# Kernel tuning notes

Measured on AMD Instinct MI355X. Metric: run time of the kernel, lower is better.

## Reference

```python
import jax, jax.numpy as jnp
import numpy as np

HIDDEN = 1024
HEADS = 16
HEAD = HIDDEN // HEADS
EXPAND = 4096
EPS = 1e-5


def layer_norm(x, g, b):
    mu = jnp.mean(x, axis=-1, keepdims=True)
    var = jnp.mean((x - mu) ** 2, axis=-1, keepdims=True)
    return (x - mu) * jax.lax.rsqrt(var + EPS) * g + b


def setup_inputs() -> dict:
    key = jax.random.key(0)
    ks = jax.random.split(key, 12)
    s = 0.02
    return {
        "x": jax.random.normal(ks[0], (4, 2048, HIDDEN), dtype=jnp.float32),
        "Wqkv": jax.random.normal(ks[1], (HIDDEN, 3 * HIDDEN), dtype=jnp.float32) * s,
        "bqkv": jnp.zeros((3 * HIDDEN,), jnp.float32),
        "Wproj": jax.random.normal(ks[2], (HIDDEN, HIDDEN), dtype=jnp.float32) * s,
        "bproj": jnp.zeros((HIDDEN,), jnp.float32),
        "W1": jax.random.normal(ks[3], (HIDDEN, EXPAND), dtype=jnp.float32) * s,
        "b1": jnp.zeros((EXPAND,), jnp.float32),
        "W2": jax.random.normal(ks[4], (EXPAND, HIDDEN), dtype=jnp.float32) * s,
        "b2": jnp.zeros((HIDDEN,), jnp.float32),
        "g1": jnp.ones((HIDDEN,), jnp.float32),
        "be1": jnp.zeros((HIDDEN,), jnp.float32),
        "g2": jnp.ones((HIDDEN,), jnp.float32),
        "be2": jnp.zeros((HIDDEN,), jnp.float32),
    }


def attention(x, Wqkv, bqkv, Wproj, bproj):
    B, L, _ = x.shape
    qkv = (x @ Wqkv + bqkv).reshape(B, L, 3, HEADS, HEAD)
    q, k, v = [qkv[:, :, i].transpose(0, 2, 1, 3) for i in range(3)]  # [B,H,L,D]
    attn = jnp.einsum("bnld,bnkd->bnlk", q, k) / np.sqrt(HEAD).astype(np.float32)
    attn = jax.nn.softmax(attn, axis=-1)
    o = jnp.einsum("bnlk,bnkd->bnld", attn, v)
    o = o.transpose(0, 2, 1, 3).reshape(B, L, HIDDEN)
    return o @ Wproj + bproj


def reference(x, Wqkv, bqkv, Wproj, bproj, W1, b1, W2, b2, g1, be1, g2, be2):
    # post-norm transformer block (pre_norm=False), dropout=0 (eval)
    h = layer_norm(x + attention(x, Wqkv, bqkv, Wproj, bproj), g1, be1)
    ff = jax.nn.gelu(h @ W1 + b1, approximate=False) @ W2 + b2
    return layer_norm(h + ff, g2, be2)
```

## Files before the change

### kernel.cpp

```cpp
#include <hip/hip_runtime.h>
#include <hip/hip_bf16.h>
#include <math.h>


typedef __bf16 bf16_t;
typedef __bf16 bf16x8 __attribute__((ext_vector_type(8)));
typedef __bf16 bf16x4 __attribute__((ext_vector_type(4)));
typedef float f32x4 __attribute__((ext_vector_type(4)));
typedef float f32x16 __attribute__((ext_vector_type(16)));

#define HID   1024
#define NHEAD 16
#define HD    64
#define EXPD  4096
#define LSEQ  2048
#define BATCH 4
#define MROWS (BATCH * LSEQ)

#if __has_builtin(__builtin_amdgcn_exp2f)
#define EXP2F __builtin_amdgcn_exp2f
#else
#define EXP2F exp2f
#endif

__device__ __forceinline__ void gld_lds16(const bf16_t* g, bf16_t* l) {
  __builtin_amdgcn_global_load_lds(
      (const __attribute__((address_space(1))) void*)g,
      (__attribute__((address_space(3))) void*)l, 16, 0, 0);
}

__device__ __forceinline__ void swap32(unsigned& a, unsigned& b) {
#if __has_builtin(__builtin_amdgcn_permlane32_swap)
  auto r = __builtin_amdgcn_permlane32_swap(a, b, false, false);
  a = r[0]; b = r[1];
#else
  bool hiL = ((threadIdx.x & 63) >= 32);
  unsigned pa = (unsigned)__shfl_xor((int)a, 32, 64);
  unsigned pb = (unsigned)__shfl_xor((int)b, 32, 64);
  unsigned na = hiL ? pb : a;
  unsigned nb = hiL ? b : pa;
  a = na; b = nb;
#endif
}

__device__ __forceinline__ unsigned pk_bf16(float lo, float hi) {
  bf16_t l = (bf16_t)lo, h = (bf16_t)hi;
  unsigned short ul, uh;
  __builtin_memcpy(&ul, &l, 2);
  __builtin_memcpy(&uh, &h, 2);
  return (unsigned)ul | ((unsigned)uh << 16);
}

__global__ __launch_bounds__(256) void cvt_bf16(const float* __restrict__ in,
                                                bf16_t* __restrict__ out, int n4) {
  int i = blockIdx.x * 256 + threadIdx.x;
  if (i >= n4) return;
  float4 v = ((const float4*)in)[i];
  bf16x4 o;
  o[0] = (bf16_t)v.x; o[1] = (bf16_t)v.y; o[2] = (bf16_t)v.z; o[3] = (bf16_t)v.w;
  ((bf16x4*)out)[i] = o;
}

__global__ __launch_bounds__(256) void transpose_cvt(const float* __restrict__ W,
                                                     bf16_t* __restrict__ Wt,
                                                     int K, int N) {
  __shared__ float tile[32][33];
  int n0 = blockIdx.x * 32, k0 = blockIdx.y * 32;
  int tx = threadIdx.x & 31, ty = threadIdx.x >> 5;
#pragma unroll
  for (int i = 0; i < 32; i += 8)
    tile[ty + i][tx] = W[(size_t)(k0 + ty + i) * N + n0 + tx];
  __syncthreads();
#pragma unroll
  for (int i = 0; i < 32; i += 8)
    Wt[(size_t)(n0 + ty + i) * K + k0 + tx] = (bf16_t)tile[tx][ty + i];
}

__global__ __launch_bounds__(256) void transpose_v(const bf16_t* __restrict__ qkvb,
                                                   bf16_t* __restrict__ vT) {
  __shared__ bf16_t tile[64][65];
  const int l0 = blockIdx.x * 64;
  const int bh = blockIdx.y;
  const int b = bh >> 4, h = bh & 15;
  const int tx = threadIdx.x & 63, ty = threadIdx.x >> 6;
  const bf16_t* src = qkvb + ((size_t)(b * LSEQ + l0)) * 3072 + 2048 + h * 64;
#pragma unroll
  for (int i = 0; i < 16; ++i) {
    int l = ty + 4 * i;
    tile[l][tx] = src[(size_t)l * 3072 + tx];
  }
  __syncthreads();
  bf16_t* dst = vT + ((size_t)bh * HD) * LSEQ + l0;
#pragma unroll
  for (int i = 0; i < 16; ++i) {
    int d = ty + 4 * i;
    dst[(size_t)d * LSEQ + tx] = tile[tx][d];
  }
}

__global__ __launch_bounds__(256) void gemm_bt(const bf16_t* __restrict__ A,
                                               const bf16_t* __restrict__ Bt,
                                               const float* __restrict__ bias,
                                               void* __restrict__ C,
                                               int M, int N, int K, int mode) {
  __shared__ bf16_t As[128 * 32];
  __shared__ bf16_t Bs[128 * 32];
  const int nbx = gridDim.x;
  int p = blockIdx.y * nbx + blockIdx.x;
  const int GM = 8;
  int group = p / (GM * nbx);
  int idx = p - group * (GM * nbx);
  const int by = group * GM + (idx & (GM - 1));
  const int bx = idx >> 3;
  const int n0 = bx * 128, m0 = by * 128;

  const int t = threadIdx.x;
  const int lane = t & 63, w = t >> 6;
  const int wr = w >> 1, wc = w & 1;
  const int quad = lane >> 4, l16 = lane & 15;

  f32x4 acc[4][4];
#pragma unroll
  for (int i = 0; i < 4; ++i)
#pragma unroll
    for (int j = 0; j < 4; ++j) acc[i][j] = (f32x4){0.f, 0.f, 0.f, 0.f};

  const int r0 = t >> 2;
  const unsigned ksw = (((unsigned)t & 3u) ^ ((unsigned)(r0 >> 1) & 3u)) * 8u;
  const unsigned offL0 = (unsigned)r0 * (unsigned)K + ksw;
  const unsigned offL1 = offL0 + 64u * (unsigned)K;

  const bf16_t* aK = A + (size_t)m0 * K;
  const bf16_t* bK = Bt + (size_t)n0 * K;

  for (int k0 = 0; k0 < K; k0 += 32) {
    gld_lds16(aK + offL0, As + t * 8);
    gld_lds16(aK + offL1, As + (t + 256) * 8);
    gld_lds16(bK + offL0, Bs + t * 8);
    gld_lds16(bK + offL1, Bs + (t + 256) * 8);
    aK += 32;
    bK += 32;
    __syncthreads();
    bf16x8 af[4], bfr[4];
#pragma unroll
    for (int i = 0; i < 4; ++i) {
      int row = wr * 64 + 16 * i + l16;
      int pos = row * 4 + (quad ^ ((row >> 1) & 3));
      af[i] = *(const bf16x8*)(As + pos * 8);
    }
#pragma unroll
    for (int j = 0; j < 4; ++j) {
      int row = wc * 64 + 16 * j + l16;
      int pos = row * 4 + (quad ^ ((row >> 1) & 3));
      bfr[j] = *(const bf16x8*)(Bs + pos * 8);
    }
#pragma unroll
    for (int i = 0; i < 4; ++i)
#pragma unroll
      for (int j = 0; j < 4; ++j)
        acc[i][j] = __builtin_amdgcn_mfma_f32_16x16x32_bf16(af[i], bfr[j], acc[i][j], 0, 0, 0);
    __syncthreads();
  }

#pragma unroll
  for (int i = 0; i < 4; ++i) {
    int rowb = m0 + wr * 64 + 16 * i + quad * 4;
#pragma unroll
    for (int j = 0; j < 4; ++j) {
      int col = n0 + wc * 64 + 16 * j + l16;
      float bv = bias[col];
#pragma unroll
      for (int r = 0; r < 4; ++r) {
        float v = acc[i][j][r] + bv;
        size_t idx = (size_t)(rowb + r) * N + col;
        if (mode == 0) {
          ((bf16_t*)C)[idx] = (bf16_t)v;
        } else if (mode == 1) {
          float u = v * (0.7978845608028654f + 0.0356774081f * v * v);
          float e = EXP2F(u * 2.885390082f);
          float th = (e - 1.f) / (e + 1.f);
          float gel = 0.5f * v * (1.f + th);
          ((bf16_t*)C)[idx] = (bf16_t)gel;
        } else {
          ((float*)C)[idx] = v;
        }
      }
    }
  }
}

__global__ __launch_bounds__(256) void attn_kernel(const bf16_t* __restrict__ qkv,
                                                   const bf16_t* __restrict__ vT,
                                                   bf16_t* __restrict__ ob) {
  __shared__ bf16_t smem[3 * 128 * 64];
  bf16_t* Ks  = smem;
  bf16_t* Vts = smem + 8192;
  bf16_t* Qs  = smem + 16384;
  const int qt = blockIdx.x, h = blockIdx.y, b = blockIdx.z;
  const int t = threadIdx.x, lane = t & 63, w = t >> 6;
  const int l32 = lane & 31, hi = lane >> 5;
  const size_t RS = 3 * HID;
  const int bh = b * NHEAD + h;

  const bf16_t* qbase = qkv + ((size_t)(b * LSEQ + qt * 128)) * RS + h * HD;
  const bf16_t* kbase = qkv + ((size_t)b * LSEQ) * RS + HID + h * HD;
  const bf16_t* vtbase = vT + (size_t)bh * HD * LSEQ;

#pragma unroll
  for (int s = 0; s < 4; ++s) {
    int l = t + s * 256;
    int r = l >> 3, c8 = l & 7;
    gld_lds16(qbase + (size_t)r * RS + ((c8 ^ (r & 7)) * 8), Qs + l * 8);
  }
  __syncthreads();

  const float sc = 0.18033688011112042f;
  bf16x8 bq[4];
  {
    int qrow = 32 * w + l32;
#pragma unroll
    for (int c = 0; c < 4; ++c) {
      int y = 2 * c + hi;
      bf16x8 q8 = *(const bf16x8*)(Qs + qrow * 64 + ((y ^ (qrow & 7)) * 8));
#pragma unroll
      for (int e = 0; e < 8; ++e) q8[e] = (bf16_t)((float)q8[e] * sc);
      bq[c] = q8;
    }
  }

  f32x16 accO[2];
#pragma unroll
  for (int dt = 0; dt < 2; ++dt)
#pragma unroll
    for (int e = 0; e < 16; ++e) accO[dt][e] = 0.f;
  float l_acc = 0.f;

  for (int kt = 0; kt < LSEQ / 128; ++kt) {
    __syncthreads();
#pragma unroll
    for (int s = 0; s < 4; ++s) {
      int l = t + s * 256;
      int r = l >> 3, c8 = l & 7;
      gld_lds16(kbase + (size_t)(kt * 128 + r) * RS + ((c8 ^ (r & 7)) * 8), Ks + l * 8);
      int rv = l >> 4, c16 = l & 15;
      gld_lds16(vtbase + (size_t)rv * LSEQ + kt * 128 + ((c16 ^ (rv & 7)) * 8), Vts + l * 8);
    }
    __syncthreads();

#pragma unroll
    for (int kt2 = 0; kt2 < 2; ++kt2) {
      f32x16 s0, s1;
#pragma unroll
      for (int e = 0; e < 16; ++e) { s0[e] = 0.f; s1[e] = 0.f; }
#pragma unroll
      for (int c = 0; c < 4; ++c) {
        int y = 2 * c + hi;
        int r0 = (2 * kt2 + 0) * 32 + l32;
        bf16x8 a0 = *(const bf16x8*)(Ks + r0 * 64 + ((y ^ (r0 & 7)) * 8));
        s0 = __builtin_amdgcn_mfma_f32_32x32x16_bf16(a0, bq[c], s0, 0, 0, 0);
        int r1 = (2 * kt2 + 1) * 32 + l32;
        bf16x8 a1 = *(const bf16x8*)(Ks + r1 * 64 + ((y ^ (r1 & 7)) * 8));
        s1 = __builtin_amdgcn_mfma_f32_32x32x16_bf16(a1, bq[c], s1, 0, 0, 0);
      }

      unsigned pf[2][2][4];
#pragma unroll
      for (int tile = 0; tile < 2; ++tile) {
        f32x16& sv = tile ? s1 : s0;
        float p[16];
#pragma unroll
        for (int e = 0; e < 16; ++e) { p[e] = EXP2F(sv[e]); l_acc += p[e]; }
        unsigned lo[4], hi_[4];
#pragma unroll
        for (int g = 0; g < 4; ++g) {
          lo[g] = pk_bf16(p[4 * g + 0], p[4 * g + 1]);
          hi_[g] = pk_bf16(p[4 * g + 2], p[4 * g + 3]);
        }
#pragma unroll
        for (int c2 = 0; c2 < 2; ++c2) {
          unsigned aL = lo[2 * c2], bL = lo[2 * c2 + 1];
          swap32(aL, bL);
          pf[tile][c2][0] = aL; pf[tile][c2][2] = bL;
          unsigned aH = hi_[2 * c2], bH = hi_[2 * c2 + 1];
          swap32(aH, bH);
          pf[tile][c2][1] = aH; pf[tile][c2][3] = bH;
        }
      }

#pragma unroll
      for (int dt = 0; dt < 2; ++dt)
#pragma unroll
        for (int tile = 0; tile < 2; ++tile)
#pragma unroll
          for (int c2 = 0; c2 < 2; ++c2) {
            int ktile = 2 * kt2 + tile;
            int c8v = ktile * 4 + c2 * 2 + hi;
            int rv = dt * 32 + l32;
            bf16x8 av = *(const bf16x8*)(Vts + rv * 128 + ((c8v ^ (rv & 7)) * 8));
            union { unsigned u[4]; bf16x8 v; } bp;
            bp.u[0] = pf[tile][c2][0]; bp.u[1] = pf[tile][c2][1];
            bp.u[2] = pf[tile][c2][2]; bp.u[3] = pf[tile][c2][3];
            accO[dt] = __builtin_amdgcn_mfma_f32_32x32x16_bf16(av, bp.v, accO[dt], 0, 0, 0);
          }
    }
  }

  l_acc += __shfl_xor(l_acc, 32, 64);
  float inv = 1.f / l_acc;

  __syncthreads();
  bf16_t* Osh = smem;
  {
    int q = 32 * w + l32;
#pragma unroll
    for (int dt = 0; dt < 2; ++dt)
#pragma unroll
      for (int e = 0; e < 16; ++e) {
        int d = dt * 32 + (e & 3) + 8 * (e >> 2) + 4 * hi;
        Osh[q * 68 + d] = (bf16_t)(accO[dt][e] * inv);
      }
  }
  __syncthreads();
#pragma unroll
  for (int s = 0; s < 4; ++s) {
    int l = t + s * 256;
    int r = l >> 3, c8 = l & 7;
    bf16x8 v = *(const bf16x8*)(Osh + r * 68 + c8 * 8);
    *(bf16x8*)(ob + ((size_t)(b * LSEQ + qt * 128 + r)) * HID + h * HD + c8 * 8) = v;
  }
}

__global__ __launch_bounds__(256) void resid_ln(const float* __restrict__ X,
                                                const float* __restrict__ Y,
                                                const float* __restrict__ g,
                                                const float* __restrict__ be,
                                                float* __restrict__ outf,
                                                bf16_t* __restrict__ outb) {
  const int row = blockIdx.x;
  const int t = threadIdx.x;
  float4 a = ((const float4*)X)[(size_t)row * 256 + t];
  float4 bvec = ((const float4*)Y)[(size_t)row * 256 + t];
  float v0 = a.x + bvec.x, v1 = a.y + bvec.y, v2 = a.z + bvec.z, v3 = a.w + bvec.w;
  float s = v0 + v1 + v2 + v3;
  float s2 = v0 * v0 + v1 * v1 + v2 * v2 + v3 * v3;
#pragma unroll
  for (int msk = 1; msk < 64; msk <<= 1) {
    s += __shfl_xor(s, msk, 64);
    s2 += __shfl_xor(s2, msk, 64);
  }
  __shared__ float red[8];
  int w = t >> 6;
  if ((t & 63) == 0) { red[w] = s; red[w + 4] = s2; }
  __syncthreads();
  s = red[0] + red[1] + red[2] + red[3];
  s2 = red[4] + red[5] + red[6] + red[7];
  float mu = s * (1.f / 1024.f);
  float var = s2 * (1.f / 1024.f) - mu * mu;
  float rstd = rsqrtf(var + 1e-5f);
  float4 gg = ((const float4*)g)[t];
  float4 bb = ((const float4*)be)[t];
  float o0 = (v0 - mu) * rstd * gg.x + bb.x;
  float o1 = (v1 - mu) * rstd * gg.y + bb.y;
  float o2 = (v2 - mu) * rstd * gg.z + bb.z;
  float o3 = (v3 - mu) * rstd * gg.w + bb.w;
  float4 o = {o0, o1, o2, o3};
  ((float4*)outf)[(size_t)row * 256 + t] = o;
  if (outb) {
    bf16x4 ob4;
    ob4[0] = (bf16_t)o0; ob4[1] = (bf16_t)o1; ob4[2] = (bf16_t)o2; ob4[3] = (bf16_t)o3;
    ((bf16x4*)outb)[(size_t)row * 256 + t] = ob4;
  }
}

extern "C" void kernel_launch(void* const* d_in, const int* in_sizes, int n_in,
                              void* d_out, int out_size, void* d_ws, size_t ws_size,
                              hipStream_t stream) {
  const float* x     = (const float*)d_in[0];
  const float* Wqkv  = (const float*)d_in[1];
  const float* bqkv  = (const float*)d_in[2];
  const float* Wproj = (const float*)d_in[3];
  const float* bproj = (const float*)d_in[4];
  const float* W1    = (const float*)d_in[5];
  const float* b1    = (const float*)d_in[6];
  const float* W2    = (const float*)d_in[7];
  const float* b2    = (const float*)d_in[8];
  const float* g1    = (const float*)d_in[9];
  const float* be1   = (const float*)d_in[10];
  const float* g2    = (const float*)d_in[11];
  const float* be2   = (const float*)d_in[12];
  float* out = (float*)d_out;

  char* ws = (char*)d_ws;
  size_t off = 0;
  auto alloc = [&](size_t bytes) -> char* {
    char* p = ws + off;
    off += (bytes + 255) & ~(size_t)255;
    return p;
  };
  bf16_t* wqkvT  = (bf16_t*)alloc((size_t)3072 * 1024 * 2);
  bf16_t* wprojT = (bf16_t*)alloc((size_t)1024 * 1024 * 2);
  bf16_t* w1T    = (bf16_t*)alloc((size_t)4096 * 1024 * 2);
  bf16_t* w2T    = (bf16_t*)alloc((size_t)1024 * 4096 * 2);
  char*   xb_ob  = alloc((size_t)MROWS * HID * 2);
  char*   qkv_ff = alloc((size_t)MROWS * EXPD * 2);
  char*   a_f2   = alloc((size_t)MROWS * HID * 4);
  float*  h      = (float*)alloc((size_t)MROWS * HID * 4);
  bf16_t* hb     = (bf16_t*)alloc((size_t)MROWS * HID * 2);

  bf16_t* xb    = (bf16_t*)xb_ob;
  bf16_t* ob    = (bf16_t*)xb_ob;
  bf16_t* qkvb  = (bf16_t*)qkv_ff;
  bf16_t* ff1b  = (bf16_t*)qkv_ff;
  float*  attnf = (float*)a_f2;
  float*  ff2f  = (float*)a_f2;
  bf16_t* vTg   = hb;

  dim3 blk(256);
  transpose_cvt<<<dim3(3072 / 32, 1024 / 32), blk, 0, stream>>>(Wqkv, wqkvT, 1024, 3072);
  transpose_cvt<<<dim3(1024 / 32, 1024 / 32), blk, 0, stream>>>(Wproj, wprojT, 1024, 1024);
  transpose_cvt<<<dim3(4096 / 32, 1024 / 32), blk, 0, stream>>>(W1, w1T, 1024, 4096);
  transpose_cvt<<<dim3(1024 / 32, 4096 / 32), blk, 0, stream>>>(W2, w2T, 4096, 1024);
  cvt_bf16<<<MROWS * HID / 4 / 256, blk, 0, stream>>>(x, xb, MROWS * HID / 4);

  gemm_bt<<<dim3(3072 / 128, MROWS / 128), blk, 0, stream>>>(xb, wqkvT, bqkv, qkvb,
                                                             MROWS, 3072, 1024, 0);
  transpose_v<<<dim3(LSEQ / 64, BATCH * NHEAD), blk, 0, stream>>>(qkvb, vTg);
  attn_kernel<<<dim3(LSEQ / 128, NHEAD, BATCH), blk, 0, stream>>>(qkvb, vTg, ob);
  gemm_bt<<<dim3(1024 / 128, MROWS / 128), blk, 0, stream>>>(ob, wprojT, bproj, attnf,
                                                             MROWS, 1024, 1024, 2);
  resid_ln<<<MROWS, blk, 0, stream>>>(x, attnf, g1, be1, h, hb);
  gemm_bt<<<dim3(4096 / 128, MROWS / 128), blk, 0, stream>>>(hb, w1T, b1, ff1b,
                                                             MROWS, 4096, 1024, 1);
  gemm_bt<<<dim3(1024 / 128, MROWS / 128), blk, 0, stream>>>(ff1b, w2T, b2, ff2f,
                                                             MROWS, 1024, 4096, 2);
  resid_ln<<<MROWS, blk, 0, stream>>>(h, ff2f, g2, be2, out, (bf16_t*)nullptr);
}
```

Before: 618.2 us.

## Replace GEMM with 4-stage pipelined 512-thread kernel using larger tiles

Replaces the single-buffered 128x128 GEMM with a templated kernel of 512 threads and 256-wide N tiles (BM 256 or 128). It keeps a 4-slot LDS ring, prefetching three K-steps ahead with async global-to-LDS loads. Explicit vmcnt waits plus one barrier per step replace the two __syncthreads per iteration, and s_setprio is raised around the MFMA block. The aim is to hide global load latency and raise arithmetic intensity. In exchange it uses much more LDS per block, which may limit occupancy, and it depends on hand-tuned waitcnt correctness.

```diff
diff --git a/kernel.cpp b/kernel.cpp
--- a/kernel.cpp
+++ b/kernel.cpp
@@ -27,6 +27,15 @@
   __builtin_amdgcn_global_load_lds(
       (const __attribute__((address_space(1))) void*)g,
       (__attribute__((address_space(3))) void*)l, 16, 0, 0);
+}
+
+template <int N>
+__device__ __forceinline__ void wait_vm() {
+  if constexpr (N == 8)      asm volatile("s_waitcnt vmcnt(8)" ::: "memory");
+  else if constexpr (N == 6) asm volatile("s_waitcnt vmcnt(6)" ::: "memory");
+  else if constexpr (N == 4) asm volatile("s_waitcnt vmcnt(4)" ::: "memory");
+  else if constexpr (N == 3) asm volatile("s_waitcnt vmcnt(3)" ::: "memory");
+  else                       asm volatile("s_waitcnt vmcnt(0)" ::: "memory");
 }
 
 __device__ __forceinline__ void swap32(unsigned& a, unsigned& b) {
@@ -98,13 +107,17 @@
   }
 }
 
-__global__ __launch_bounds__(256) void gemm_bt(const bf16_t* __restrict__ A,
-                                               const bf16_t* __restrict__ Bt,
-                                               const float* __restrict__ bias,
-                                               void* __restrict__ C,
-                                               int M, int N, int K, int mode) {
-  __shared__ bf16_t As[128 * 32];
-  __shared__ bf16_t Bs[128 * 32];
+template <int BM>
+__global__ __launch_bounds__(512, 2) void gemm_p(const bf16_t* __restrict__ A,
+                                                 const bf16_t* __restrict__ Bt,
+                                                 const float* __restrict__ bias,
+                                                 void* __restrict__ C,
+                                                 int M, int N, int K, int mode) {
+  constexpr int MI = BM / 32;
+  constexpr int LOADS = (BM == 256) ? 4 : 3;
+  __shared__ bf16_t As[4 * BM * 32];
+  __shared__ bf16_t Bs[4 * 256 * 32];
+
   const int nbx = gridDim.x;
   int p = blockIdx.y * nbx + blockIdx.x;
   const int GM = 8;
@@ -112,59 +125,101 @@
   int idx = p - group * (GM * nbx);
   const int by = group * GM + (idx & (GM - 1));
   const int bx = idx >> 3;
-  const int n0 = bx * 128, m0 = by * 128;
+  const int n0 = bx * 256, m0 = by * BM;
 
   const int t = threadIdx.x;
   const int lane = t & 63, w = t >> 6;
-  const int wr = w >> 1, wc = w & 1;
+  const int wr = w >> 2, wc = w & 3;
   const int quad = lane >> 4, l16 = lane & 15;
 
-  f32x4 acc[4][4];
-#pragma unroll
-  for (int i = 0; i < 4; ++i)
+  f32x4 acc[MI][4];
+#pragma unroll
+  for (int i = 0; i < MI; ++i)
 #pragma unroll
     for (int j = 0; j < 4; ++j) acc[i][j] = (f32x4){0.f, 0.f, 0.f, 0.f};
 
   const int r0 = t >> 2;
   const unsigned ksw = (((unsigned)t & 3u) ^ ((unsigned)(r0 >> 1) & 3u)) * 8u;
-  const unsigned offL0 = (unsigned)r0 * (unsigned)K + ksw;
-  const unsigned offL1 = offL0 + 64u * (unsigned)K;
-
-  const bf16_t* aK = A + (size_t)m0 * K;
-  const bf16_t* bK = Bt + (size_t)n0 * K;
-
-  for (int k0 = 0; k0 < K; k0 += 32) {
-    gld_lds16(aK + offL0, As + t * 8);
-    gld_lds16(aK + offL1, As + (t + 256) * 8);
-    gld_lds16(bK + offL0, Bs + t * 8);
-    gld_lds16(bK + offL1, Bs + (t + 256) * 8);
-    aK += 32;
-    bK += 32;
-    __syncthreads();
-    bf16x8 af[4], bfr[4];
-#pragma unroll
-    for (int i = 0; i < 4; ++i) {
-      int row = wr * 64 + 16 * i + l16;
-      int pos = row * 4 + (quad ^ ((row >> 1) & 3));
-      af[i] = *(const bf16x8*)(As + pos * 8);
-    }
-#pragma unroll
-    for (int j = 0; j < 4; ++j) {
-      int row = wc * 64 + 16 * j + l16;
-      int pos = row * 4 + (quad ^ ((row >> 1) & 3));
-      bfr[j] = *(const bf16x8*)(Bs + pos * 8);
-    }
-#pragma unroll
-    for (int i = 0; i < 4; ++i)
+  const unsigned offR0 = (unsigned)r0 * (unsigned)K + ksw;
+  const unsigned off128 = offR0 + 128u * (unsigned)K;
+
+  const bf16_t* aB = A + (size_t)m0 * K;
+  const bf16_t* bB = Bt + (size_t)n0 * K;
+
+  unsigned aoff[MI], boff[4];
+#pragma unroll
+  for (int i = 0; i < MI; ++i) {
+    int row = wr * (BM / 2) + 16 * i + l16;
+    aoff[i] = (unsigned)(row * 32 + (quad ^ ((row >> 1) & 3)) * 8);
+  }
+#pragma unroll
+  for (int j = 0; j < 4; ++j) {
+    int row = wc * 64 + 16 * j + l16;
+    boff[j] = (unsigned)(row * 32 + (quad ^ ((row >> 1) & 3)) * 8);
+  }
+
+  auto stage = [&](int slot, int kk) {
+    bf16_t* Asl = As + slot * (BM * 32);
+    bf16_t* Bsl = Bs + slot * (256 * 32);
+    const bf16_t* aS = aB + kk;
+    const bf16_t* bS = bB + kk;
+    gld_lds16(aS + offR0, Asl + t * 8);
+    if constexpr (BM == 256) gld_lds16(aS + off128, Asl + (t + 512) * 8);
+    gld_lds16(bS + offR0, Bsl + t * 8);
+    gld_lds16(bS + off128, Bsl + (t + 512) * 8);
+  };
+
+  auto compute = [&](int slot) {
+    const bf16_t* Asl = As + slot * (BM * 32);
+    const bf16_t* Bsl = Bs + slot * (256 * 32);
+    bf16x8 af[MI], bfr[4];
+#pragma unroll
+    for (int i = 0; i < MI; ++i) af[i] = *(const bf16x8*)(Asl + aoff[i]);
+#pragma unroll
+    for (int j = 0; j < 4; ++j) bfr[j] = *(const bf16x8*)(Bsl + boff[j]);
+    __builtin_amdgcn_s_setprio(1);
+#pragma unroll
+    for (int i = 0; i < MI; ++i)
 #pragma unroll
       for (int j = 0; j < 4; ++j)
         acc[i][j] = __builtin_amdgcn_mfma_f32_16x16x32_bf16(af[i], bfr[j], acc[i][j], 0, 0, 0);
-    __syncthreads();
-  }
-
-#pragma unroll
-  for (int i = 0; i < 4; ++i) {
-    int rowb = m0 + wr * 64 + 16 * i + quad * 4;
+    __builtin_amdgcn_s_setprio(0);
+  };
+
+  const int NT = K >> 5;
+
+  stage(0, 0);
+  stage(1, 32);
+  stage(2, 64);
+  int kk = 96;
+
+  int kt = 0;
+  for (; kt < NT - 3; ++kt) {
+    wait_vm<2 * LOADS>();
+    __builtin_amdgcn_s_barrier();
+    asm volatile("" ::: "memory");
+    stage((kt + 3) & 3, kk);
+    kk += 32;
+    compute(kt & 3);
+  }
+  wait_vm<2 * LOADS>();
+  __builtin_amdgcn_s_barrier();
+  asm volatile("" ::: "memory");
+  compute(kt & 3);
+  ++kt;
+  wait_vm<LOADS>();
+  __builtin_amdgcn_s_barrier();
+  asm volatile("" ::: "memory");
+  compute(kt & 3);
+  ++kt;
+  wait_vm<0>();
+  __builtin_amdgcn_s_barrier();
+  asm volatile("" ::: "memory");
+  compute(kt & 3);
+
+#pragma unroll
+  for (int i = 0; i < MI; ++i) {
+    int rowb = m0 + wr * (BM / 2) + 16 * i + quad * 4;
 #pragma unroll
     for (int j = 0; j < 4; ++j) {
       int col = n0 + wc * 64 + 16 * j + l16;
@@ -416,22 +471,23 @@
   bf16_t* vTg   = hb;
 
   dim3 blk(256);
+  dim3 blk512(512);
   transpose_cvt<<<dim3(3072 / 32, 1024 / 32), blk, 0, stream>>>(Wqkv, wqkvT, 1024, 3072);
   transpose_cvt<<<dim3(1024 / 32, 1024 / 32), blk, 0, stream>>>(Wproj, wprojT, 1024, 1024);
   transpose_cvt<<<dim3(4096 / 32, 1024 / 32), blk, 0, stream>>>(W1, w1T, 1024, 4096);
   transpose_cvt<<<dim3(1024 / 32, 4096 / 32), blk, 0, stream>>>(W2, w2T, 4096, 1024);
   cvt_bf16<<<MROWS * HID / 4 / 256, blk, 0, stream>>>(x, xb, MROWS * HID / 4);
 
-  gemm_bt<<<dim3(3072 / 128, MROWS / 128), blk, 0, stream>>>(xb, wqkvT, bqkv, qkvb,
-                                                             MROWS, 3072, 1024, 0);
+  gemm_p<256><<<dim3(3072 / 256, MROWS / 256), blk512, 0, stream>>>(xb, wqkvT, bqkv, qkvb,
+                                                                    MROWS, 3072, 1024, 0);
   transpose_v<<<dim3(LSEQ / 64, BATCH * NHEAD), blk, 0, stream>>>(qkvb, vTg);
   attn_kernel<<<dim3(LSEQ / 128, NHEAD, BATCH), blk, 0, stream>>>(qkvb, vTg, ob);
-  gemm_bt<<<dim3(1024 / 128, MROWS / 128), blk, 0, stream>>>(ob, wprojT, bproj, attnf,
-                                                             MROWS, 1024, 1024, 2);
+  gemm_p<128><<<dim3(1024 / 256, MROWS / 128), blk512, 0, stream>>>(ob, wprojT, bproj, attnf,
+                                                                    MROWS, 1024, 1024, 2);
   resid_ln<<<MROWS, blk, 0, stream>>>(x, attnf, g1, be1, h, hb);
-  gemm_bt<<<dim3(4096 / 128, MROWS / 128), blk, 0, stream>>>(hb, w1T, b1, ff1b,
-                                                             MROWS, 4096, 1024, 1);
-  gemm_bt<<<dim3(1024 / 128, MROWS / 128), blk, 0, stream>>>(ff1b, w2T, b2, ff2f,
-                                                             MROWS, 1024, 4096, 2);
+  gemm_p<256><<<dim3(4096 / 256, MROWS / 256), blk512, 0, stream>>>(hb, w1T, b1, ff1b,
+                                                                    MROWS, 4096, 1024, 1);
+  gemm_p<128><<<dim3(1024 / 256, MROWS / 128), blk512, 0, stream>>>(ff1b, w2T, b2, ff2f,
+                                                                    MROWS, 1024, 4096, 2);
   resid_ln<<<MROWS, blk, 0, stream>>>(h, ff2f, g2, be2, out, (bf16_t*)nullptr);
 }
```

Result: no change. 630.5 us (+2.0%).

## Triple-buffer GEMM LDS loads with vmcnt waits and wider 128x256 tiles

Applied to the files above, without the earlier changes.

Turns the GEMM into a template that keeps three LDS stages, prefetching two k-tiles ahead with global_load_lds and waiting on vmcnt counts instead of draining at every iteration. It also precomputes the swizzled LDS offsets, raises wave priority around the MFMA block, and runs the QKV and FFN1 GEMMs with 512-thread 128x256 tiles. The goal is to hide global-load latency behind MFMA work and reuse each A tile across more columns. The cost is three times the LDS per block, which limits occupancy, and the hand-written waitcnt logic is fragile if the compiler issues other vector memory ops.

```diff
diff --git a/kernel.cpp b/kernel.cpp
--- a/kernel.cpp
+++ b/kernel.cpp
@@ -27,6 +27,18 @@
   __builtin_amdgcn_global_load_lds(
       (const __attribute__((address_space(1))) void*)g,
       (__attribute__((address_space(3))) void*)l, 16, 0, 0);
+}
+
+__device__ __forceinline__ void vmwait(int n) {
+  if (n == 4)      asm volatile("s_waitcnt vmcnt(4)" ::: "memory");
+  else if (n == 3) asm volatile("s_waitcnt vmcnt(3)" ::: "memory");
+  else if (n == 0) asm volatile("s_waitcnt vmcnt(0)" ::: "memory");
+}
+
+__device__ __forceinline__ void block_bar() {
+  asm volatile("" ::: "memory");
+  __builtin_amdgcn_s_barrier();
+  asm volatile("" ::: "memory");
 }
 
 __device__ __forceinline__ void swap32(unsigned& a, unsigned& b) {
@@ -98,13 +110,21 @@
   }
 }
 
-__global__ __launch_bounds__(256) void gemm_bt(const bf16_t* __restrict__ A,
-                                               const bf16_t* __restrict__ Bt,
-                                               const float* __restrict__ bias,
-                                               void* __restrict__ C,
-                                               int M, int N, int K, int mode) {
-  __shared__ bf16_t As[128 * 32];
-  __shared__ bf16_t Bs[128 * 32];
+template <int BM, int BN, int NTHR>
+__global__ __launch_bounds__(NTHR, (NTHR == 512 ? 4 : 3))
+void gemm_k(const bf16_t* __restrict__ A,
+            const bf16_t* __restrict__ Bt,
+            const float* __restrict__ bias,
+            void* __restrict__ C,
+            int M, int N, int K, int mode) {
+  constexpr int WC = (NTHR / 64) / 2;
+  constexpr int AL = BM * 4 / NTHR;
+  constexpr int BL = BN * 4 / NTHR;
+  constexpr int LOADS = AL + BL;
+  constexpr int RSTEP = NTHR >> 2;
+  __shared__ bf16_t As[3 * BM * 32];
+  __shared__ bf16_t Bs[3 * BN * 32];
+
   const int nbx = gridDim.x;
   int p = blockIdx.y * nbx + blockIdx.x;
   const int GM = 8;
@@ -112,11 +132,11 @@
   int idx = p - group * (GM * nbx);
   const int by = group * GM + (idx & (GM - 1));
   const int bx = idx >> 3;
-  const int n0 = bx * 128, m0 = by * 128;
+  const int n0 = bx * BN, m0 = by * BM;
 
   const int t = threadIdx.x;
   const int lane = t & 63, w = t >> 6;
-  const int wr = w >> 1, wc = w & 1;
+  const int wr = w / WC, wc = w % WC;
   const int quad = lane >> 4, l16 = lane & 15;
 
   f32x4 acc[4][4];
@@ -127,39 +147,67 @@
 
   const int r0 = t >> 2;
   const unsigned ksw = (((unsigned)t & 3u) ^ ((unsigned)(r0 >> 1) & 3u)) * 8u;
-  const unsigned offL0 = (unsigned)r0 * (unsigned)K + ksw;
-  const unsigned offL1 = offL0 + 64u * (unsigned)K;
-
-  const bf16_t* aK = A + (size_t)m0 * K;
-  const bf16_t* bK = Bt + (size_t)n0 * K;
-
-  for (int k0 = 0; k0 < K; k0 += 32) {
-    gld_lds16(aK + offL0, As + t * 8);
-    gld_lds16(aK + offL1, As + (t + 256) * 8);
-    gld_lds16(bK + offL0, Bs + t * 8);
-    gld_lds16(bK + offL1, Bs + (t + 256) * 8);
-    aK += 32;
-    bK += 32;
-    __syncthreads();
+  const unsigned offR0 = (unsigned)r0 * (unsigned)K + ksw;
+
+  const bf16_t* aB = A + (size_t)m0 * K;
+  const bf16_t* bB = Bt + (size_t)n0 * K;
+
+  unsigned aoff[4], boff[4];
+#pragma unroll
+  for (int i = 0; i < 4; ++i) {
+    int row = wr * 64 + 16 * i + l16;
+    aoff[i] = (unsigned)(row * 32 + (quad ^ ((row >> 1) & 3)) * 8);
+  }
+#pragma unroll
+  for (int j = 0; j < 4; ++j) {
+    int row = wc * 64 + 16 * j + l16;
+    boff[j] = (unsigned)(row * 32 + (quad ^ ((row >> 1) & 3)) * 8);
+  }
+
+  auto stage = [&](int slot, int kk) {
+    bf16_t* Asl = As + slot * (BM * 32);
+    bf16_t* Bsl = Bs + slot * (BN * 32);
+    const bf16_t* aS = aB + kk;
+    const bf16_t* bS = bB + kk;
+#pragma unroll
+    for (int a = 0; a < AL; ++a)
+      gld_lds16(aS + offR0 + (size_t)a * RSTEP * K, Asl + (t + a * NTHR) * 8);
+#pragma unroll
+    for (int b = 0; b < BL; ++b)
+      gld_lds16(bS + offR0 + (size_t)b * RSTEP * K, Bsl + (t + b * NTHR) * 8);
+  };
+
+  const int NT = K >> 5;
+
+  stage(0, 0);
+  stage(1, 32);
+  vmwait(LOADS);
+  block_bar();
+
+  int cs = 0;
+  for (int kt = 0; kt < NT; ++kt) {
+    if (kt < NT - 2) {
+      int ss = cs == 0 ? 2 : cs - 1;
+      stage(ss, (kt + 2) * 32);
+    }
+    const bf16_t* Asl = As + cs * (BM * 32);
+    const bf16_t* Bsl = Bs + cs * (BN * 32);
     bf16x8 af[4], bfr[4];
 #pragma unroll
-    for (int i = 0; i < 4; ++i) {
-      int row = wr * 64 + 16 * i + l16;
-      int pos = row * 4 + (quad ^ ((row >> 1) & 3));
-      af[i] = *(const bf16x8*)(As + pos * 8);
-    }
-#pragma unroll
-    for (int j = 0; j < 4; ++j) {
-      int row = wc * 64 + 16 * j + l16;
-      int pos = row * 4 + (quad ^ ((row >> 1) & 3));
-      bfr[j] = *(const bf16x8*)(Bs + pos * 8);
-    }
+    for (int i = 0; i < 4; ++i) af[i] = *(const bf16x8*)(Asl + aoff[i]);
+#pragma unroll
+    for (int j = 0; j < 4; ++j) bfr[j] = *(const bf16x8*)(Bsl + boff[j]);
+    __builtin_amdgcn_s_setprio(1);
 #pragma unroll
     for (int i = 0; i < 4; ++i)
 #pragma unroll
       for (int j = 0; j < 4; ++j)
         acc[i][j] = __builtin_amdgcn_mfma_f32_16x16x32_bf16(af[i], bfr[j], acc[i][j], 0, 0, 0);
-    __syncthreads();
+    __builtin_amdgcn_s_setprio(0);
+    if (kt < NT - 2)      vmwait(LOADS);
+    else if (kt == NT - 2) vmwait(0);
+    if (kt < NT - 1) block_bar();
+    cs = cs == 2 ? 0 : cs + 1;
   }
 
 #pragma unroll
@@ -416,22 +464,23 @@
   bf16_t* vTg   = hb;
 
   dim3 blk(256);
+  dim3 blk512(512);
   transpose_cvt<<<dim3(3072 / 32, 1024 / 32), blk, 0, stream>>>(Wqkv, wqkvT, 1024, 3072);
   transpose_cvt<<<dim3(1024 / 32, 1024 / 32), blk, 0, stream>>>(Wproj, wprojT, 1024, 1024);
   transpose_cvt<<<dim3(4096 / 32, 1024 / 32), blk, 0, stream>>>(W1, w1T, 1024, 4096);
   transpose_cvt<<<dim3(1024 / 32, 4096 / 32), blk, 0, stream>>>(W2, w2T, 4096, 1024);
   cvt_bf16<<<MROWS * HID / 4 / 256, blk, 0, stream>>>(x, xb, MROWS * HID / 4);
 
-  gemm_bt<<<dim3(3072 / 128, MROWS / 128), blk, 0, stream>>>(xb, wqkvT, bqkv, qkvb,
-                                                             MROWS, 3072, 1024, 0);
+  gemm_k<128, 256, 512><<<dim3(3072 / 256, MROWS / 128), blk512, 0, stream>>>(
+      xb, wqkvT, bqkv, qkvb, MROWS, 3072, 1024, 0);
   transpose_v<<<dim3(LSEQ / 64, BATCH * NHEAD), blk, 0, stream>>>(qkvb, vTg);
   attn_kernel<<<dim3(LSEQ / 128, NHEAD, BATCH), blk, 0, stream>>>(qkvb, vTg, ob);
-  gemm_bt<<<dim3(1024 / 128, MROWS / 128), blk, 0, stream>>>(ob, wprojT, bproj, attnf,
-                                                             MROWS, 1024, 1024, 2);
+  gemm_k<128, 128, 256><<<dim3(1024 / 128, MROWS / 128), blk, 0, stream>>>(
+      ob, wprojT, bproj, attnf, MROWS, 1024, 1024, 2);
   resid_ln<<<MROWS, blk, 0, stream>>>(x, attnf, g1, be1, h, hb);
-  gemm_bt<<<dim3(4096 / 128, MROWS / 128), blk, 0, stream>>>(hb, w1T, b1, ff1b,
-                                                             MROWS, 4096, 1024, 1);
-  gemm_bt<<<dim3(1024 / 128, MROWS / 128), blk, 0, stream>>>(ff1b, w2T, b2, ff2f,
-                                                             MROWS, 1024, 4096, 2);
+  gemm_k<128, 256, 512><<<dim3(4096 / 256, MROWS / 128), blk512, 0, stream>>>(
+      hb, w1T, b1, ff1b, MROWS, 4096, 1024, 1);
+  gemm_k<128, 128, 256><<<dim3(1024 / 128, MROWS / 128), blk, 0, stream>>>(
+      ff1b, w2T, b2, ff2f, MROWS, 1024, 4096, 2);
   resid_ln<<<MROWS, blk, 0, stream>>>(h, ff2f, g2, be2, out, (bf16_t*)nullptr);
 }
```

Measured after the change: 571.7 us. 1.08x faster.
